# Optimization experiments

Hardware: AMD Instinct MI355X
Metric: run time of the kernel (lower is better)

## Reference

```python
import math
import jax, jax.numpy as jnp
import numpy as np

B, S, D, H, KV = 2, 2048, 1024, 16, 4
HD = D // H  # 64
ROPE_BASE = 10000.0
RMS_EPS = 1.1920929e-07  # torch.finfo(float32).eps, F.rms_norm default


def setup_inputs() -> dict:
    key = jax.random.key(0)
    ks = jax.random.split(key, 5)
    x = jax.random.normal(ks[0], (B, S, D), jnp.float32)
    Wq = jax.random.normal(ks[1], (D, D), jnp.float32) * 0.02
    Wk = jax.random.normal(ks[2], (KV * HD, D), jnp.float32) * 0.02
    Wv = jax.random.normal(ks[3], (KV * HD, D), jnp.float32) * 0.02
    Wproj = jax.random.normal(ks[4], (D, D), jnp.float32) * 0.02
    q_gain = jnp.ones((H,), jnp.float32)  # qk_gain_init = 1.0
    return {"x": x, "Wq": Wq, "Wk": Wk, "Wv": Wv, "Wproj": Wproj, "q_gain": q_gain}


def _rms_norm(t):
    # F.rms_norm with no weight: t * rsqrt(mean(t^2) + eps)
    return t * jax.lax.rsqrt(jnp.mean(t * t, axis=-1, keepdims=True) + RMS_EPS)


def _rope(t, cos, sin):
    half = t.shape[-1] // 2
    t1, t2 = t[..., :half], t[..., half:]
    return jnp.concatenate([t1 * cos + t2 * sin, t1 * -sin + t2 * cos], axis=-1)


def reference(x, Wq, Wk, Wv, Wproj, q_gain):
    bsz, seqlen, dim = x.shape
    hd = dim // H
    # QKV projections (Linear weight layout [out, in])
    q = (x @ Wq.T).reshape(bsz, seqlen, H, hd).transpose(0, 2, 1, 3)    # [B,H,S,hd]
    k = (x @ Wk.T).reshape(bsz, seqlen, KV, hd).transpose(0, 2, 1, 3)   # [B,KV,S,hd]
    v = (x @ Wv.T).reshape(bsz, seqlen, KV, hd).transpose(0, 2, 1, 3)
    # per-head RMSNorm on q/k (no learned weight)
    q = _rms_norm(q)
    k = _rms_norm(k)
    # RoPE tables
    inv_freq = 1.0 / (ROPE_BASE ** (jnp.arange(0, hd, 2, dtype=jnp.float32) / hd))
    t = jnp.arange(seqlen, dtype=jnp.float32)
    freqs = t[:, None] * inv_freq[None, :]                              # [S, hd/2]
    cos = jnp.cos(freqs)[None, None]                                    # [1,1,S,hd/2]
    sin = jnp.sin(freqs)[None, None]
    q = _rope(q, cos, sin)
    k = _rope(k, cos, sin)
    # learned per-head query gain
    q = q * q_gain[None, :, None, None]
    # GQA: repeat_interleave kv heads to full head count
    rep = H // KV
    k = jnp.repeat(k, rep, axis=1)                                      # [B,H,S,hd]
    v = jnp.repeat(v, rep, axis=1)
    # causal SDPA, scale = 1/sqrt(head_dim)
    scores = jnp.einsum("bhqd,bhkd->bhqk", q, k) * (1.0 / math.sqrt(hd))
    causal = jnp.tril(jnp.ones((seqlen, seqlen), bool))
    scores = jnp.where(causal[None, None], scores, jnp.finfo(scores.dtype).min)
    attn = jax.nn.softmax(scores, axis=-1)
    y = jnp.einsum("bhqk,bhkd->bhqd", attn, v)
    y = y.transpose(0, 2, 1, 3).reshape(bsz, seqlen, dim)
    return y @ Wproj.T
```

## Files before the change

### kernel.cpp

```cpp
#include <hip/hip_runtime.h>

typedef unsigned short u16;
typedef __bf16 bf16_t;
typedef bf16_t bf16x8 __attribute__((ext_vector_type(8)));
typedef float f32x4 __attribute__((ext_vector_type(4)));
typedef u16 u16x8 __attribute__((ext_vector_type(8)));
typedef u16 u16x4 __attribute__((ext_vector_type(4)));

__device__ __forceinline__ u16 f2bf(float f) {
  unsigned u = __float_as_uint(f);
  u += 0x7fffu + ((u >> 16) & 1u);
  return (u16)(u >> 16);
}

__device__ __forceinline__ float bf2f(u16 u) {
  return __uint_as_float((unsigned)u << 16);
}

__device__ __forceinline__ unsigned cvtpk(float lo, float hi) {
  unsigned r;
  asm("v_cvt_pk_bf16_f32 %0, %1, %2" : "=v"(r) : "v"(lo), "v"(hi));
  return r;
}

__device__ __forceinline__ f32x4 mfma16(bf16x8 a, bf16x8 b, f32x4 c) {
  return __builtin_amdgcn_mfma_f32_16x16x32_bf16(a, b, c, 0, 0, 0);
}

__device__ __forceinline__ void gl2lds16(const u16* g, u16* l) {
  __builtin_amdgcn_global_load_lds(
      (__attribute__((address_space(1))) void*)(u16*)g,
      (__attribute__((address_space(3))) void*)l, 16, 0, 0);
}

__device__ __forceinline__ void cast8(const float* __restrict__ in,
                                      u16* __restrict__ out, int i) {
  float4 a = *(const float4*)&in[i];
  float4 b = *(const float4*)&in[i + 4];
  uint4 o;
  o.x = cvtpk(a.x, a.y);
  o.y = cvtpk(a.z, a.w);
  o.z = cvtpk(b.x, b.y);
  o.w = cvtpk(b.z, b.w);
  *(uint4*)&out[i] = o;
}

__global__ __launch_bounds__(256) void megacast(
    const float* __restrict__ x, const float* __restrict__ Wq,
    const float* __restrict__ Wk, const float* __restrict__ Wv,
    const float* __restrict__ Wp, u16* __restrict__ xb,
    u16* __restrict__ wallb, u16* __restrict__ wpb,
    float2* __restrict__ tbl) {
  const int blk = blockIdx.x;
  const int tid = threadIdx.x;
  if (blk < 2048) {
    cast8(x, xb, (blk * 256 + tid) * 8);
  } else if (blk < 2560) {
    cast8(Wq, wallb, ((blk - 2048) * 256 + tid) * 8);
  } else if (blk < 2688) {
    cast8(Wk, wallb + 1048576, ((blk - 2560) * 256 + tid) * 8);
  } else if (blk < 2816) {
    cast8(Wv, wallb + 1310720, ((blk - 2688) * 256 + tid) * 8);
  } else if (blk < 3328) {
    cast8(Wp, wpb, ((blk - 2816) * 256 + tid) * 8);
  } else {
    const int idx = (blk - 3328) * 256 + tid;
    const int s = idx >> 5, i = idx & 31;
    float inv = exp2f(-(float)i * (13.287712379549449f / 32.0f));
    float fr = (float)s * inv;
    float sn, cs;
    sincosf(fr, &sn, &cs);
    tbl[idx] = make_float2(cs, sn);
  }
}

template <int BM, int BN, bool O16>
__global__ __launch_bounds__(256) void gemm_bt(const u16* __restrict__ A,
                                               const u16* __restrict__ B,
                                               void* __restrict__ Cv,
                                               int M, int N, int K) {
  constexpr int FM = BM / 32;
  constexpr int FN = BN / 32;
  constexpr int NL = (BM + BN) / 32;
  __shared__ __align__(16) u16 As[2][BM][64];
  __shared__ __align__(16) u16 Bs[2][BN][64];
  const int tid = threadIdx.x;
  const int lane = tid & 63;
  const int lg = lane >> 4, li = lane & 15;
  const int wave = tid >> 6;
  const int wr = (wave >> 1) * (BM / 2), wc = (wave & 1) * (BN / 2);
  const int m0 = blockIdx.y * BM, n0 = blockIdx.x * BN;

  const int s_r = tid >> 3;
  const int s_c = (tid & 7) ^ ((tid >> 3) & 7);
  const int rdsw = li & 7;

  auto GSTAGE = [&](int buf, int k0) {
    const u16* ga = &A[(size_t)(m0 + s_r) * K + k0 + s_c * 8];
#pragma unroll
    for (int i = 0; i < BM / 32; i++)
      gl2lds16(ga + (size_t)(i * 32) * K, &As[buf][i * 32][0] + (size_t)tid * 8);
    const u16* gb = &B[(size_t)(n0 + s_r) * K + k0 + s_c * 8];
#pragma unroll
    for (int i = 0; i < BN / 32; i++)
      gl2lds16(gb + (size_t)(i * 32) * K, &Bs[buf][i * 32][0] + (size_t)tid * 8);
  };

  const f32x4 fz = {0.f, 0.f, 0.f, 0.f};
  f32x4 acc[FM][FN];
#pragma unroll
  for (int i = 0; i < FM; i++)
#pragma unroll
    for (int j = 0; j < FN; j++) acc[i][j] = fz;

  GSTAGE(0, 0);
  int buf = 0;
  const int nk = K >> 6;
  for (int t = 0; t < nk; ++t) {
    if (t + 1 < nk) {
      GSTAGE(buf ^ 1, (t + 1) * 64);
      if constexpr (NL == 6)
        asm volatile("s_waitcnt vmcnt(6)" ::: "memory");
      else if constexpr (NL == 7)
        asm volatile("s_waitcnt vmcnt(7)" ::: "memory");
      else
        asm volatile("s_waitcnt vmcnt(8)" ::: "memory");
    } else {
      asm volatile("s_waitcnt vmcnt(0)" ::: "memory");
    }
    __builtin_amdgcn_s_barrier();
#pragma unroll
    for (int kk = 0; kk < 2; kk++) {
      bf16x8 af[FM], bfr[FN];
#pragma unroll
      for (int i = 0; i < FM; i++)
        af[i] = *(const bf16x8*)&As[buf][wr + i * 16 + li]
                                   [((kk * 4 + lg) ^ rdsw) * 8];
#pragma unroll
      for (int j = 0; j < FN; j++)
        bfr[j] = *(const bf16x8*)&Bs[buf][wc + j * 16 + li]
                                    [((kk * 4 + lg) ^ rdsw) * 8];
      __builtin_amdgcn_s_setprio(1);
#pragma unroll
      for (int i = 0; i < FM; i++)
#pragma unroll
        for (int j = 0; j < FN; j++) acc[i][j] = mfma16(af[i], bfr[j], acc[i][j]);
      __builtin_amdgcn_s_setprio(0);
    }
    __builtin_amdgcn_s_barrier();
    buf ^= 1;
  }
#pragma unroll
  for (int i = 0; i < FM; i++)
#pragma unroll
    for (int j = 0; j < FN; j++)
#pragma unroll
      for (int r = 0; r < 4; r++) {
        const size_t idx =
            (size_t)(m0 + wr + i * 16 + lg * 4 + r) * N + n0 + wc + j * 16 + li;
        if constexpr (O16)
          ((u16*)Cv)[idx] = f2bf(acc[i][j][r]);
        else
          ((float*)Cv)[idx] = acc[i][j][r];
      }
}

__global__ __launch_bounds__(256) void posttrans(const u16* __restrict__ qf,
                                                 const float* __restrict__ qg,
                                                 u16* __restrict__ qhb,
                                                 u16* __restrict__ khb,
                                                 u16* __restrict__ vtb, int S,
                                                 const float2* __restrict__ tbl) {
  const int idx = blockIdx.x;
  const int tid = threadIdx.x;
  if (idx < 20480) {
    const int h = idx >> 10;
    const int rowblk = idx & 1023;
    const int w = tid >> 6;
    const int t = tid & 63;
    const int row = rowblk * 4 + w;
    const bool isq = h < 16;
    const int col = isq ? h * 64 : 1024 + (h - 16) * 64;
    const float v = bf2f(qf[(size_t)row * 1536 + col + t]);
    float ss = v * v;
#pragma unroll
    for (int m = 1; m < 64; m <<= 1) ss += __shfl_xor(ss, m);
    const float vn = v * rsqrtf(ss * (1.0f / 64.0f) + 1.1920929e-07f);
    const float partner = __shfl_xor(vn, 32);
    const int b = row / S;
    const int s = row - b * S;
    const float2 cs2 = tbl[s * 32 + (t & 31)];
    float o = (t < 32) ? (vn * cs2.x + partner * cs2.y)
                       : (vn * cs2.x - partner * cs2.y);
    if (isq) {
      o *= 0.18033688011112042f * qg[h];
      qhb[((size_t)(b * 16 + h) * S + s) * 64 + t] = f2bf(o);
    } else {
      khb[((size_t)(b * 4 + (h - 16)) * S + s) * 64 + t] = f2bf(o);
    }
  } else {
    const int blk = idx - 20480;
    const int sc = blk & 7;
    const int kv = (blk >> 3) & 3;
    const int b = blk >> 5;
    __shared__ u16 T[256][66];
    const int dcol = tid & 63;
    const int w = tid >> 6;
    const u16* src =
        qf + (size_t)(b * S + sc * 256) * 1536 + 1280 + kv * 64 + dcol;
#pragma unroll 4
    for (int i = 0; i < 64; ++i) {
      const int sl = i * 4 + w;
      T[sl][dcol] = src[(size_t)sl * 1536];
    }
    __syncthreads();
    u16* dst = vtb + (size_t)((b * 4 + kv) * 64) * S + sc * 256;
    const int l = tid & 63;
#pragma unroll 4
    for (int i = 0; i < 16; ++i) {
      const int drow = i * 4 + w;
      u16x4 v4;
      v4[0] = T[l * 4 + 0][drow];
      v4[1] = T[l * 4 + 1][drow];
      v4[2] = T[l * 4 + 2][drow];
      v4[3] = T[l * 4 + 3][drow];
      *(u16x4*)(dst + (size_t)drow * S + l * 4) = v4;
    }
  }
}

__global__ __launch_bounds__(256) void attn13(const u16* __restrict__ qh,
                                              const u16* __restrict__ kh,
                                              const u16* __restrict__ vt,
                                              const float* __restrict__ qg,
                                              u16* __restrict__ y, int S) {
  const int bh = blockIdx.x & 31;
  const int g = blockIdx.x >> 5;
  const int d = g & 7, u = g >> 3;
  const int qb = (u == 0) ? 31 - d : (u == 1) ? 16 + d : (u == 2) ? 15 - d : d;
  const int h = bh & 15, b = bh >> 4;
  const int kvh = h >> 2;
  const int tid = threadIdx.x;
  const int wave = tid >> 6;
  const int lane = tid & 63;
  const int lg = lane >> 4, li = lane & 15;
  const int q0 = qb * 64 + wave * 16;
  const int qrow = q0 + li;
  const float mrow = 11.541560327111707f * fabsf(qg[h]);

  const u16* qp = qh + ((size_t)(b * 16 + h) * S + q0) * 64;
  const u16* kp = kh + (size_t)(b * 4 + kvh) * S * 64;
  const u16* vp = vt + (size_t)(b * 4 + kvh) * 64 * S;

  __shared__ __align__(16) u16 Ks[2][64][64];
  __shared__ __align__(16) u16 Vs[2][64][64];

  const int s_r0 = tid >> 3;
  const int s_rp = (s_r0 & ~24) | ((s_r0 & 8) << 1) | ((s_r0 & 16) >> 1);
  const int s_c = (tid & 7) ^ ((tid >> 3) & 7);
  const int rdsw = li & 7;
  const f32x4 minit = {-mrow, -mrow, -mrow, -mrow};
  const f32x4 fz = {0.f, 0.f, 0.f, 0.f};
  const u16x8 ones_u = {0x3F80, 0x3F80, 0x3F80, 0x3F80,
                        0x3F80, 0x3F80, 0x3F80, 0x3F80};
  const bf16x8 onesb = *(const bf16x8*)&ones_u;

#define STAGE(buf, kb)                                                        \
  {                                                                           \
    const u16* gk = kp + (size_t)((kb) + s_rp) * 64 + s_c * 8;                \
    gl2lds16(gk, &Ks[buf][0][0] + (size_t)tid * 8);                           \
    gl2lds16(gk + (size_t)32 * 64, &Ks[buf][32][0] + (size_t)tid * 8);        \
    const u16* gv = vp + (size_t)s_r0 * S + (kb) + s_c * 8;                   \
    gl2lds16(gv, &Vs[buf][0][0] + (size_t)tid * 8);                           \
    gl2lds16(gv + (size_t)32 * S, &Vs[buf][32][0] + (size_t)tid * 8);         \
  }

  STAGE(0, 0)
  const bf16x8 qf0 = *(const bf16x8*)&qp[li * 64 + lg * 8];
  const bf16x8 qf1 = *(const bf16x8*)&qp[li * 64 + 32 + lg * 8];

  f32x4 o[4];
#pragma unroll
  for (int j = 0; j < 4; j++) o[j] = fz;
  f32x4 lsum = fz;

  int buf = 0;
  for (int tt = 0; tt <= qb; ++tt) {
    if (tt < qb) {
      STAGE(buf ^ 1, (tt + 1) * 64)
      asm volatile("s_waitcnt vmcnt(4)" ::: "memory");
    } else {
      asm volatile("s_waitcnt vmcnt(0)" ::: "memory");
    }
    __builtin_amdgcn_s_barrier();
    const int kb = tt * 64;
    f32x4 s[4];
    __builtin_amdgcn_s_setprio(1);
#pragma unroll
    for (int t = 0; t < 4; t++) {
      const bf16x8 ka =
          *(const bf16x8*)&Ks[buf][t * 16 + li][((lg) ^ rdsw) * 8];
      const bf16x8 kc =
          *(const bf16x8*)&Ks[buf][t * 16 + li][((lg + 4) ^ rdsw) * 8];
      s[t] = mfma16(ka, qf0, minit);
      s[t] = mfma16(kc, qf1, s[t]);
    }
    __builtin_amdgcn_s_setprio(0);
    float pv[16];
    if (tt < qb) {
#pragma unroll
      for (int t = 0; t < 4; t++)
#pragma unroll
        for (int r = 0; r < 4; r++) pv[t * 4 + r] = exp2f(s[t][r]);
    } else {
#pragma unroll
      for (int t = 0; t < 4; t++)
#pragma unroll
        for (int r = 0; r < 4; r++) {
          const int key = kb + ((t >> 1) << 5) + ((lg & 2) << 3) +
                          ((t & 1) << 3) + ((lg & 1) << 2) + r;
          pv[t * 4 + r] = exp2f(key > qrow ? -1e30f : s[t][r]);
        }
    }
    unsigned w0 = cvtpk(pv[0], pv[1]),   w1 = cvtpk(pv[2], pv[3]);
    unsigned w2 = cvtpk(pv[4], pv[5]),   w3 = cvtpk(pv[6], pv[7]);
    unsigned w4 = cvtpk(pv[8], pv[9]),   w5 = cvtpk(pv[10], pv[11]);
    unsigned w6 = cvtpk(pv[12], pv[13]), w7 = cvtpk(pv[14], pv[15]);
    asm("v_permlane16_swap_b32 %0, %1" : "+v"(w0), "+v"(w2));
    asm("v_permlane16_swap_b32 %0, %1" : "+v"(w1), "+v"(w3));
    asm("v_permlane16_swap_b32 %0, %1" : "+v"(w4), "+v"(w6));
    asm("v_permlane16_swap_b32 %0, %1" : "+v"(w5), "+v"(w7));
    uint4 pb0u = {w0, w1, w2, w3};
    uint4 pb1u = {w4, w5, w6, w7};
    const bf16x8 pb0 = *(const bf16x8*)&pb0u;
    const bf16x8 pb1 = *(const bf16x8*)&pb1u;
    __builtin_amdgcn_s_setprio(1);
#pragma unroll
    for (int j = 0; j < 4; j++) {
      const bf16x8 v0 =
          *(const bf16x8*)&Vs[buf][j * 16 + li][((lg) ^ rdsw) * 8];
      const bf16x8 v1 =
          *(const bf16x8*)&Vs[buf][j * 16 + li][((lg + 4) ^ rdsw) * 8];
      o[j] = mfma16(v0, pb0, o[j]);
      o[j] = mfma16(v1, pb1, o[j]);
    }
    lsum = mfma16(onesb, pb0, lsum);
    lsum = mfma16(onesb, pb1, lsum);
    __builtin_amdgcn_s_setprio(0);
    __builtin_amdgcn_s_barrier();
    buf ^= 1;
  }
#undef STAGE
  const float linv = 1.0f / lsum[0];
  u16* yp = &y[((size_t)(b * S + q0 + li)) * 1024 + h * 64];
#pragma unroll
  for (int j = 0; j < 4; j++) {
    uint2 wo;
    wo.x = cvtpk(o[j][0] * linv, o[j][1] * linv);
    wo.y = cvtpk(o[j][2] * linv, o[j][3] * linv);
    *(uint2*)(yp + j * 16 + lg * 4) = wo;
  }
}

extern "C" void kernel_launch(void* const* d_in, const int* in_sizes, int n_in,
                              void* d_out, int out_size, void* d_ws, size_t ws_size,
                              hipStream_t stream) {
  const float* x  = (const float*)d_in[0];
  const float* Wq = (const float*)d_in[1];
  const float* Wk = (const float*)d_in[2];
  const float* Wv = (const float*)d_in[3];
  const float* Wp = (const float*)d_in[4];
  const float* qg = (const float*)d_in[5];
  float* out = (float*)d_out;

  const int S = 2048;
  char* ws = (char*)d_ws;
  u16*    xb    = (u16*)(ws + 0);
  u16*    wallb = (u16*)(ws + 8388608);
  u16*    wpb   = (u16*)(ws + 11534336);
  float2* tbl   = (float2*)(ws + 13631488);
  u16*    qf    = (u16*)(ws + 14155776);
  u16*    qhb   = (u16*)(ws + 26738688);
  u16*    khb   = (u16*)(ws + 35127296);
  u16*    vtb   = (u16*)(ws + 37224448);
  u16*    yb    = (u16*)(ws + 39321600);
  if (ws_size < 47710208) return;

  megacast<<<3584, 256, 0, stream>>>(x, Wq, Wk, Wv, Wp, xb, wallb, wpb, tbl);

  gemm_bt<128, 64, true><<<dim3(24, 32), 256, 0, stream>>>(xb, wallb, qf,
                                                           4096, 1536, 1024);

  posttrans<<<20544, 256, 0, stream>>>(qf, qg, qhb, khb, vtb, S, tbl);

  attn13<<<1024, 256, 0, stream>>>(qhb, khb, vtb, qg, yb, S);

  gemm_bt<64, 128, false><<<dim3(8, 64), 256, 0, stream>>>(yb, wpb, out,
                                                           4096, 1024, 1024);
}
```

Measured before the change: 112.6 us.

## Fuse RMSNorm, RoPE, and V transpose into QKV GEMM epilogue

Replaces the standalone QKV GEMM plus posttrans kernel with one gemm_qkv kernel. Its epilogue computes the per-head RMS norm (a cross-wave reduction through LDS), applies RoPE and the query scale, and writes the transposed V directly. This removes the bf16 qf intermediate round-trip and a kernel launch. Separately, both GEMMs now remap block IDs so consecutive blocks are spread across the 8 XCDs, aiming at better L2 locality. The cost is a heavier epilogue with extra LDS traffic and syncs.

```diff
diff --git a/kernel.cpp b/kernel.cpp
--- a/kernel.cpp
+++ b/kernel.cpp
@@ -5,16 +5,11 @@
 typedef bf16_t bf16x8 __attribute__((ext_vector_type(8)));
 typedef float f32x4 __attribute__((ext_vector_type(4)));
 typedef u16 u16x8 __attribute__((ext_vector_type(8)));
-typedef u16 u16x4 __attribute__((ext_vector_type(4)));
 
 __device__ __forceinline__ u16 f2bf(float f) {
   unsigned u = __float_as_uint(f);
   u += 0x7fffu + ((u >> 16) & 1u);
   return (u16)(u >> 16);
-}
-
-__device__ __forceinline__ float bf2f(u16 u) {
-  return __uint_as_float((unsigned)u << 16);
 }
 
 __device__ __forceinline__ unsigned cvtpk(float lo, float hi) {
@@ -74,7 +69,7 @@
   }
 }
 
-template <int BM, int BN, bool O16>
+template <int BM, int BN, int NTN, bool O16>
 __global__ __launch_bounds__(256) void gemm_bt(const u16* __restrict__ A,
                                                const u16* __restrict__ B,
                                                void* __restrict__ Cv,
@@ -89,7 +84,8 @@
   const int lg = lane >> 4, li = lane & 15;
   const int wave = tid >> 6;
   const int wr = (wave >> 1) * (BM / 2), wc = (wave & 1) * (BN / 2);
-  const int m0 = blockIdx.y * BM, n0 = blockIdx.x * BN;
+  const int wid = (blockIdx.x & 7) * (gridDim.x >> 3) + (blockIdx.x >> 3);
+  const int m0 = (wid / NTN) * BM, n0 = (wid % NTN) * BN;
 
   const int s_r = tid >> 3;
   const int s_c = (tid & 7) ^ ((tid >> 3) & 7);
@@ -121,8 +117,6 @@
       GSTAGE(buf ^ 1, (t + 1) * 64);
       if constexpr (NL == 6)
         asm volatile("s_waitcnt vmcnt(6)" ::: "memory");
-      else if constexpr (NL == 7)
-        asm volatile("s_waitcnt vmcnt(7)" ::: "memory");
       else
         asm volatile("s_waitcnt vmcnt(8)" ::: "memory");
     } else {
@@ -165,66 +159,153 @@
       }
 }
 
-__global__ __launch_bounds__(256) void posttrans(const u16* __restrict__ qf,
-                                                 const float* __restrict__ qg,
-                                                 u16* __restrict__ qhb,
-                                                 u16* __restrict__ khb,
-                                                 u16* __restrict__ vtb, int S,
-                                                 const float2* __restrict__ tbl) {
-  const int idx = blockIdx.x;
+__global__ __launch_bounds__(256) void gemm_qkv(const u16* __restrict__ A,
+                                                const u16* __restrict__ B,
+                                                const float* __restrict__ qg,
+                                                u16* __restrict__ qhb,
+                                                u16* __restrict__ khb,
+                                                u16* __restrict__ vtb,
+                                                const float2* __restrict__ tbl) {
+  const int K = 1024, S = 2048;
+  __shared__ __align__(16) u16 As[2][128][64];
+  __shared__ __align__(16) u16 Bs[2][64][64];
   const int tid = threadIdx.x;
-  if (idx < 20480) {
-    const int h = idx >> 10;
-    const int rowblk = idx & 1023;
-    const int w = tid >> 6;
-    const int t = tid & 63;
-    const int row = rowblk * 4 + w;
-    const bool isq = h < 16;
-    const int col = isq ? h * 64 : 1024 + (h - 16) * 64;
-    const float v = bf2f(qf[(size_t)row * 1536 + col + t]);
-    float ss = v * v;
-#pragma unroll
-    for (int m = 1; m < 64; m <<= 1) ss += __shfl_xor(ss, m);
-    const float vn = v * rsqrtf(ss * (1.0f / 64.0f) + 1.1920929e-07f);
-    const float partner = __shfl_xor(vn, 32);
-    const int b = row / S;
-    const int s = row - b * S;
-    const float2 cs2 = tbl[s * 32 + (t & 31)];
-    float o = (t < 32) ? (vn * cs2.x + partner * cs2.y)
-                       : (vn * cs2.x - partner * cs2.y);
-    if (isq) {
-      o *= 0.18033688011112042f * qg[h];
-      qhb[((size_t)(b * 16 + h) * S + s) * 64 + t] = f2bf(o);
+  const int lane = tid & 63;
+  const int lg = lane >> 4, li = lane & 15;
+  const int wave = tid >> 6;
+  const int wr = (wave >> 1) * 64, wc = (wave & 1) * 32;
+  const int wid = (blockIdx.x & 7) * 96 + (blockIdx.x >> 3);
+  const int mt = wid / 24;
+  const int ntile = wid - mt * 24;
+  const int m0 = mt * 128;
+
+  const int s_r = tid >> 3;
+  const int s_c = (tid & 7) ^ ((tid >> 3) & 7);
+  const int rdsw = li & 7;
+
+  auto GSTAGE = [&](int buf, int k0) {
+    const u16* ga = &A[(size_t)(m0 + s_r) * K + k0 + s_c * 8];
+#pragma unroll
+    for (int i = 0; i < 4; i++)
+      gl2lds16(ga + (size_t)(i * 32) * K, &As[buf][i * 32][0] + (size_t)tid * 8);
+    const u16* gb = &B[(size_t)(ntile * 64 + s_r) * K + k0 + s_c * 8];
+#pragma unroll
+    for (int i = 0; i < 2; i++)
+      gl2lds16(gb + (size_t)(i * 32) * K, &Bs[buf][i * 32][0] + (size_t)tid * 8);
+  };
+
+  const f32x4 fz = {0.f, 0.f, 0.f, 0.f};
+  f32x4 acc[4][2];
+#pragma unroll
+  for (int i = 0; i < 4; i++)
+#pragma unroll
+    for (int j = 0; j < 2; j++) acc[i][j] = fz;
+
+  GSTAGE(0, 0);
+  int buf = 0;
+  for (int t = 0; t < 16; ++t) {
+    if (t + 1 < 16) {
+      GSTAGE(buf ^ 1, (t + 1) * 64);
+      asm volatile("s_waitcnt vmcnt(6)" ::: "memory");
     } else {
-      khb[((size_t)(b * 4 + (h - 16)) * S + s) * 64 + t] = f2bf(o);
-    }
+      asm volatile("s_waitcnt vmcnt(0)" ::: "memory");
+    }
+    __builtin_amdgcn_s_barrier();
+#pragma unroll
+    for (int kk = 0; kk < 2; kk++) {
+      bf16x8 af[4], bfr[2];
+#pragma unroll
+      for (int i = 0; i < 4; i++)
+        af[i] = *(const bf16x8*)&As[buf][wr + i * 16 + li]
+                                   [((kk * 4 + lg) ^ rdsw) * 8];
+#pragma unroll
+      for (int j = 0; j < 2; j++)
+        bfr[j] = *(const bf16x8*)&Bs[buf][wc + j * 16 + li]
+                                    [((kk * 4 + lg) ^ rdsw) * 8];
+      __builtin_amdgcn_s_setprio(1);
+#pragma unroll
+      for (int i = 0; i < 4; i++)
+#pragma unroll
+        for (int j = 0; j < 2; j++) acc[i][j] = mfma16(af[i], bfr[j], acc[i][j]);
+      __builtin_amdgcn_s_setprio(0);
+    }
+    __builtin_amdgcn_s_barrier();
+    buf ^= 1;
+  }
+
+  if (ntile < 20) {
+    float* acc_t = (float*)&As[0][0][0];
+    float* sw = (float*)&Bs[0][0][0];
+    float ssq[4][4];
+#pragma unroll
+    for (int i = 0; i < 4; i++)
+#pragma unroll
+      for (int r = 0; r < 4; r++) {
+        float s2 = acc[i][0][r] * acc[i][0][r] + acc[i][1][r] * acc[i][1][r];
+        s2 += __shfl_xor(s2, 1);
+        s2 += __shfl_xor(s2, 2);
+        s2 += __shfl_xor(s2, 4);
+        s2 += __shfl_xor(s2, 8);
+        ssq[i][r] = s2;
+        const int rowidx = i * 16 + lg * 4 + r;
+        if (li == 0) sw[wave * 64 + rowidx] = s2;
+#pragma unroll
+        for (int j = 0; j < 2; j++)
+          acc_t[wave * 2048 + rowidx * 32 + j * 16 + li] = acc[i][j][r];
+      }
+    __syncthreads();
+    const int pw = wave ^ 1;
+    const float qsc =
+        (ntile < 16) ? 0.18033688011112042f * qg[ntile] : 1.0f;
+#pragma unroll
+    for (int i = 0; i < 4; i++)
+#pragma unroll
+      for (int r = 0; r < 4; r++) {
+        const int rowidx = i * 16 + lg * 4 + r;
+        const float stot = ssq[i][r] + sw[pw * 64 + rowidx];
+        const float rn = rsqrtf(stot * (1.0f / 64.0f) + 1.1920929e-07f);
+        const int grow = m0 + wr + rowidx;
+        const int srow = grow & 2047;
+        const int bb = grow >> 11;
+#pragma unroll
+        for (int j = 0; j < 2; j++) {
+          const int fi = j * 16 + li;
+          const float2 cs2 = tbl[srow * 32 + fi];
+          const float vn = acc[i][j][r] * rn;
+          const float pvn = acc_t[pw * 2048 + rowidx * 32 + fi] * rn;
+          float o = (wc == 0) ? (vn * cs2.x + pvn * cs2.y)
+                              : (vn * cs2.x - pvn * cs2.y);
+          o *= qsc;
+          const int col = wc + fi;
+          if (ntile < 16)
+            qhb[((size_t)(bb * 16 + ntile) * S + srow) * 64 + col] = f2bf(o);
+          else
+            khb[((size_t)(bb * 4 + (ntile - 16)) * S + srow) * 64 + col] =
+                f2bf(o);
+        }
+      }
   } else {
-    const int blk = idx - 20480;
-    const int sc = blk & 7;
-    const int kv = (blk >> 3) & 3;
-    const int b = blk >> 5;
-    __shared__ u16 T[256][66];
-    const int dcol = tid & 63;
-    const int w = tid >> 6;
-    const u16* src =
-        qf + (size_t)(b * S + sc * 256) * 1536 + 1280 + kv * 64 + dcol;
-#pragma unroll 4
-    for (int i = 0; i < 64; ++i) {
-      const int sl = i * 4 + w;
-      T[sl][dcol] = src[(size_t)sl * 1536];
-    }
+    u16* T = (u16*)&As[0][0][0];
+#pragma unroll
+    for (int i = 0; i < 4; i++)
+#pragma unroll
+      for (int j = 0; j < 2; j++)
+#pragma unroll
+        for (int r = 0; r < 4; r++)
+          T[(wr + i * 16 + lg * 4 + r) * 67 + wc + j * 16 + li] =
+              f2bf(acc[i][j][r]);
     __syncthreads();
-    u16* dst = vtb + (size_t)((b * 4 + kv) * 64) * S + sc * 256;
-    const int l = tid & 63;
-#pragma unroll 4
-    for (int i = 0; i < 16; ++i) {
-      const int drow = i * 4 + w;
-      u16x4 v4;
-      v4[0] = T[l * 4 + 0][drow];
-      v4[1] = T[l * 4 + 1][drow];
-      v4[2] = T[l * 4 + 2][drow];
-      v4[3] = T[l * 4 + 3][drow];
-      *(u16x4*)(dst + (size_t)drow * S + l * 4) = v4;
+    const int kv = ntile - 20;
+    const int d = tid >> 2;
+    const int sq = (tid & 3) * 32;
+    const int bb = m0 >> 11;
+    const int s0 = (m0 & 2047) + sq;
+    unsigned* dst = (unsigned*)(vtb + ((size_t)(bb * 4 + kv) * 64 + d) * S + s0);
+#pragma unroll
+    for (int k2 = 0; k2 < 16; k2++) {
+      unsigned lo = T[(sq + 2 * k2) * 67 + d];
+      unsigned hi = T[(sq + 2 * k2 + 1) * 67 + d];
+      dst[k2] = lo | (hi << 16);
     }
   }
 }
@@ -379,22 +460,18 @@
   u16*    wallb = (u16*)(ws + 8388608);
   u16*    wpb   = (u16*)(ws + 11534336);
   float2* tbl   = (float2*)(ws + 13631488);
-  u16*    qf    = (u16*)(ws + 14155776);
-  u16*    qhb   = (u16*)(ws + 26738688);
-  u16*    khb   = (u16*)(ws + 35127296);
-  u16*    vtb   = (u16*)(ws + 37224448);
-  u16*    yb    = (u16*)(ws + 39321600);
-  if (ws_size < 47710208) return;
+  u16*    qhb   = (u16*)(ws + 14155776);
+  u16*    khb   = (u16*)(ws + 22544384);
+  u16*    vtb   = (u16*)(ws + 24641536);
+  u16*    yb    = (u16*)(ws + 26738688);
+  if (ws_size < 35127296) return;
 
   megacast<<<3584, 256, 0, stream>>>(x, Wq, Wk, Wv, Wp, xb, wallb, wpb, tbl);
 
-  gemm_bt<128, 64, true><<<dim3(24, 32), 256, 0, stream>>>(xb, wallb, qf,
-                                                           4096, 1536, 1024);
-
-  posttrans<<<20544, 256, 0, stream>>>(qf, qg, qhb, khb, vtb, S, tbl);
+  gemm_qkv<<<768, 256, 0, stream>>>(xb, wallb, qg, qhb, khb, vtb, tbl);
 
   attn13<<<1024, 256, 0, stream>>>(qhb, khb, vtb, qg, yb, S);
 
-  gemm_bt<64, 128, false><<<dim3(8, 64), 256, 0, stream>>>(yb, wpb, out,
-                                                           4096, 1024, 1024);
-}
+  gemm_bt<64, 128, 8, false><<<512, 256, 0, stream>>>(yb, wpb, out,
+                                                      4096, 1024, 1024);
+}
```

Measured after the change: 90.24 us, median of 3. 19.9% less time.
